# Kernel tuning notes

Hardware: AMD Instinct MI355X
Metric: run time of the kernel (lower is better)

Reference implementation:

```python
import jax, jax.numpy as jnp
import numpy as np

DIM = 384
H = 12
HD = DIM // H  # 32
GROUPS = 6
K = 7
EPS = 1e-5


def layernorm(x, g, b):
    m = x.mean(-1, keepdims=True)
    v = x.var(-1, keepdims=True)
    return (x - m) * jax.lax.rsqrt(v + EPS) * g + b


def setup_inputs() -> dict:
    key = jax.random.key(0)
    ks = jax.random.split(key, 12)
    B, S = 8, 4096
    s = 0.02
    inp = {
        "x": jax.random.normal(ks[0], (B, S, DIM), jnp.float32),
        # grouped Conv1d: weight (out=384, in_per_group=64, k=7)
        "conv_w": jax.random.normal(ks[1], (DIM, DIM // GROUPS, K), jnp.float32) * s,
        "conv_b": jnp.zeros((DIM,), jnp.float32),
        "q_w": jax.random.normal(ks[2], (DIM, DIM), jnp.float32) * s,
        "q_b": jnp.zeros((DIM,), jnp.float32),
        "k_w": jax.random.normal(ks[3], (DIM, DIM), jnp.float32) * s,
        "k_b": jnp.zeros((DIM,), jnp.float32),
        "v_w": jax.random.normal(ks[4], (DIM, DIM), jnp.float32) * s,
        "v_b": jnp.zeros((DIM,), jnp.float32),
        "g_w": jax.random.normal(ks[5], (DIM, DIM), jnp.float32) * s,
        "g_b": jnp.zeros((DIM,), jnp.float32),
        "decay": jnp.ones((1, H, 1, HD), jnp.float32) * 0.85,
        "ln1_g": jnp.ones((DIM,), jnp.float32),
        "ln1_b": jnp.zeros((DIM,), jnp.float32),
        "w1": jax.random.normal(ks[6], (DIM, 2 * DIM), jnp.float32) * s,
        "b1": jnp.zeros((2 * DIM,), jnp.float32),
        "w2": jax.random.normal(ks[7], (2 * DIM, DIM), jnp.float32) * s,
        "b2": jnp.zeros((DIM,), jnp.float32),
        "ln2_g": jnp.ones((DIM,), jnp.float32),
        "ln2_b": jnp.zeros((DIM,), jnp.float32),
    }
    return inp


def reference(x, conv_w, conv_b, q_w, q_b, k_w, k_b, v_w, v_b, g_w, g_b,
              decay, ln1_g, ln1_b, w1, b1, w2, b2, ln2_g, ln2_b):
    b, s, d = x.shape
    # grouped depth-blocked conv over time (torch Conv1d, pad=3, groups=6)
    xc = jax.lax.conv_general_dilated(
        x.transpose(0, 2, 1), conv_w, window_strides=(1,), padding=((3, 3),),
        feature_group_count=GROUPS, dimension_numbers=("NCH", "OIH", "NCH"))
    xc = (xc + conv_b[None, :, None]).transpose(0, 2, 1)
    xc = jax.nn.silu(xc)

    def heads(y):  # (b,s,d) -> (b,h,s,hd)
        return y.reshape(b, s, H, HD).transpose(0, 2, 1, 3)

    q = heads(xc @ q_w + q_b)
    k = heads(xc @ k_w + k_b)
    v = heads(xc @ v_w + v_b)
    g = heads(jax.nn.sigmoid(xc @ g_w + g_b))
    v_gated = v * g

    # Fallback recurrence: state = state * mean(sigmoid(decay)) + v_t (x) k_t;
    # output reads only diag(state) -> collapses to a per-dim decayed cumsum of v*k.
    lam = jnp.mean(jax.nn.sigmoid(decay))  # scalar (mean over h,d of expanded w)
    u = v_gated * k                        # (b,h,s,hd)
    u_t = u.transpose(2, 0, 1, 3)          # (s,b,h,hd)

    def step(carry, ut):
        c = carry * lam + ut
        return c, c

    _, diag = jax.lax.scan(step, jnp.zeros((b, H, HD), x.dtype), u_t)
    out = q * diag.transpose(1, 2, 0, 3)   # (b,h,s,hd)

    x_mem = out.transpose(0, 2, 1, 3).reshape(b, s, d)
    h = layernorm(x_mem, ln1_g, ln1_b)
    h = jax.nn.silu(h @ w1 + b1) @ w2 + b2
    return layernorm(h + x, ln2_g, ln2_b)
```

## Files before the change

kernel.cpp:

```cpp
#include <hip/hip_runtime.h>
#include <hip/hip_bf16.h>

#define DIMD 384
#define SEQL 4096
#define NBATCH 8
#define NTOK (NBATCH*SEQL)

typedef float f32x4 __attribute__((ext_vector_type(4)));
typedef short s16x8 __attribute__((ext_vector_type(8)));
typedef unsigned short u16;
typedef __hip_bfloat16 bf16;

__device__ __forceinline__ float sigf(float x){ return 1.f/(1.f+__expf(-x)); }

typedef __attribute__((address_space(3))) void lds_void;
typedef const __attribute__((address_space(1))) void glb_void;
__device__ __forceinline__ void gl_lds16(const void* g, void* l) {
  __builtin_amdgcn_global_load_lds((glb_void*)g, (lds_void*)l, 16, 0, 0);
}

#define OFF_LAM   0ul
#define OFF_WQ    4096ul
#define OFF_CW    (OFF_WQ + 1179648ul)
#define OFF_W1T   (OFF_CW + 344064ul)
#define OFF_W2T   (OFF_W1T + 589824ul)
#define OFF_XC    4194304ul
#define OFF_Q     (OFF_XC + 25165824ul)
#define OFF_U     (OFF_XC + 50331648ul)
#define OFF_AI    OFF_U
#define OFF_H     (OFF_U + 50331648ul)

__global__ void k_prep_w(const float* __restrict__ qw, const float* __restrict__ kw,
                         const float* __restrict__ vw, const float* __restrict__ gw,
                         const float* __restrict__ cw, const float* __restrict__ w1,
                         const float* __restrict__ w2,
                         bf16* __restrict__ wqt, bf16* __restrict__ cwt,
                         bf16* __restrict__ w1t, bf16* __restrict__ w2t) {
  const int total = 589824 + 172032 + 294912 + 294912;
  for (int j = blockIdx.x*blockDim.x + threadIdx.x; j < total; j += gridDim.x*blockDim.x) {
    if (j < 589824) {
      int n = j / 384, k = j % 384;
      int mat = n / 384;
      int np = n % 384;
      const float* W = (mat==0)?qw:(mat==1)?kw:(mat==2)?vw:gw;
      wqt[(size_t)n*384 + k] = __float2bfloat16(W[(size_t)k*384 + np]);
    } else if (j < 589824 + 172032) {
      int jj = j - 589824;
      int o = jj / 448, k = jj % 448;
      int kap = k >> 6, i = k & 63;
      cwt[(size_t)o*448 + k] = __float2bfloat16(cw[((size_t)o*64 + i)*7 + kap]);
    } else if (j < 589824 + 172032 + 294912) {
      int jj = j - (589824 + 172032);
      int n = jj / 384, k = jj % 384;
      w1t[(size_t)n*384 + k] = __float2bfloat16(w1[(size_t)k*768 + n]);
    } else {
      int jj = j - (589824 + 172032 + 294912);
      int n = jj / 768, k = jj % 768;
      w2t[(size_t)n*768 + k] = __float2bfloat16(w2[(size_t)k*384 + n]);
    }
  }
}

__global__ void k_prep_lam(const float* __restrict__ decay, float* __restrict__ lam) {
  __shared__ float red[6];
  int t = threadIdx.x;
  float v = sigf(decay[t]);
  for (int off = 32; off; off >>= 1) v += __shfl_xor(v, off, 64);
  if ((t & 63) == 0) red[t >> 6] = v;
  __syncthreads();
  if (t == 0) {
    float s = 0.f;
    for (int i = 0; i < 6; ++i) s += red[i];
    lam[0] = s * (1.f/384.f);
  }
}

__global__ __launch_bounds__(256) void k_conv(const float* __restrict__ x, const float* __restrict__ cb,
                                              const bf16* __restrict__ cwt, bf16* __restrict__ xc) {
  int id = blockIdx.x;
  int g = id % 6, st = (id/6) & 31, b = id / 192;
  int s0 = st * 128;
  __shared__ u16 xls[134*72];
  __shared__ u16 wls[64*456];
  int tid = threadIdx.x;
  for (int r0 = 0; r0 < 144; r0 += 16) {
    int row = r0 + (tid >> 4);
    if (row < 134) {
      int col = (tid & 15) * 4;
      int s = s0 - 3 + row;
      float4 v = make_float4(0.f,0.f,0.f,0.f);
      if (s >= 0 && s < SEQL)
        v = *reinterpret_cast<const float4*>(x + ((size_t)(b*SEQL + s))*DIMD + g*64 + col);
      u16* dst = &xls[row*72 + col];
      bf16 t0 = __float2bfloat16(v.x); dst[0] = *reinterpret_cast<u16*>(&t0);
      bf16 t1 = __float2bfloat16(v.y); dst[1] = *reinterpret_cast<u16*>(&t1);
      bf16 t2 = __float2bfloat16(v.z); dst[2] = *reinterpret_cast<u16*>(&t2);
      bf16 t3 = __float2bfloat16(v.w); dst[3] = *reinterpret_cast<u16*>(&t3);
    }
  }
  for (int i0 = 0; i0 < 28672; i0 += 1024) {
    int i = i0 + tid*4;
    int o = i / 448, k = i % 448;
    *reinterpret_cast<uint2*>(&wls[o*456 + k]) =
      *reinterpret_cast<const uint2*>(cwt + ((size_t)(g*64 + o))*448 + k);
  }
  __syncthreads();
  int w = tid >> 6, l = tid & 63, l15 = l & 15, lh = l >> 4;
  f32x4 zz = {0.f,0.f,0.f,0.f};
  f32x4 acc[2][4];
  for (int i=0;i<2;++i) for (int jn=0;jn<4;++jn) acc[i][jn]=zz;
  for (int kap = 0; kap < 7; ++kap) {
#pragma unroll
    for (int ic = 0; ic < 2; ++ic) {
      s16x8 a0 = *reinterpret_cast<const s16x8*>(&xls[(w*32 +  0 + l15 + kap)*72 + ic*32 + lh*8]);
      s16x8 a1 = *reinterpret_cast<const s16x8*>(&xls[(w*32 + 16 + l15 + kap)*72 + ic*32 + lh*8]);
#pragma unroll
      for (int nf = 0; nf < 4; ++nf) {
        s16x8 bfr = *reinterpret_cast<const s16x8*>(&wls[(nf*16 + l15)*456 + kap*64 + ic*32 + lh*8]);
        acc[0][nf] = __builtin_amdgcn_mfma_f32_16x16x32_bf16(a0, bfr, acc[0][nf], 0,0,0);
        acc[1][nf] = __builtin_amdgcn_mfma_f32_16x16x32_bf16(a1, bfr, acc[1][nf], 0,0,0);
      }
    }
  }
#pragma unroll
  for (int nf = 0; nf < 4; ++nf) {
    int ch = g*64 + nf*16 + l15;
    float bias = cb[ch];
#pragma unroll
    for (int mf = 0; mf < 2; ++mf) {
#pragma unroll
      for (int r = 0; r < 4; ++r) {
        int m = w*32 + mf*16 + lh*4 + r;
        float v = acc[mf][nf][r] + bias;
        v = v * sigf(v);
        xc[((size_t)(b*SEQL + s0 + m))*DIMD + ch] = __float2bfloat16(v);
      }
    }
  }
}

__global__ __launch_bounds__(256) void k_qkvg(const bf16* __restrict__ xc, const bf16* __restrict__ wt,
    const float* __restrict__ qb, const float* __restrict__ kb,
    const float* __restrict__ vb, const float* __restrict__ gb,
    bf16* __restrict__ qout, bf16* __restrict__ uout) {
  int raw = blockIdx.x;
  int vv = (raw & 7)*384 + (raw >> 3);
  int mt = vv / 12, ct = vv % 12;
  int m0 = mt*128, c0 = ct*32;
  __shared__ __align__(16) u16 smem[16384];
  u16* als = smem;
  int tid = threadIdx.x, w = tid >> 6, l = tid & 63, l15 = l & 15, lh = l >> 4;
  f32x4 zz = {0.f,0.f,0.f,0.f};
  f32x4 acc[8][2];
#pragma unroll
  for (int i=0;i<8;++i){ acc[i][0]=zz; acc[i][1]=zz; }
  const bf16* b0p = wt + ((size_t)(w*384 + c0 + l15))*384 + lh*8;
  const bf16* b1p = b0p + (size_t)16*384;
  for (int kc = 0; kc < 3; ++kc) {
#pragma unroll
    for (int p = 0; p < 8; ++p) {
      int off16 = p*256 + tid;
      int row = off16 >> 4, slot = off16 & 15;
      int sslot = slot ^ (row & 7);
      gl_lds16(xc + ((size_t)(m0+row))*DIMD + kc*128 + sslot*8,
               (char*)als + off16*16);
    }
    __syncthreads();
#pragma unroll
    for (int kk = 0; kk < 4; ++kk) {
      int ko = kc*128 + kk*32;
      s16x8 bf0 = *reinterpret_cast<const s16x8*>(b0p + ko);
      s16x8 bf1 = *reinterpret_cast<const s16x8*>(b1p + ko);
#pragma unroll
      for (int mf = 0; mf < 8; ++mf) {
        s16x8 af = *reinterpret_cast<const s16x8*>(
            &als[(mf*16 + l15)*128 + (((kk*4 + lh) ^ (l15 & 7))*8)]);
        acc[mf][0] = __builtin_amdgcn_mfma_f32_16x16x32_bf16(af, bf0, acc[mf][0], 0,0,0);
        acc[mf][1] = __builtin_amdgcn_mfma_f32_16x16x32_bf16(af, bf1, acc[mf][1], 0,0,0);
      }
    }
    __syncthreads();
  }
  const float* bp = (w==0)?qb:(w==1)?kb:(w==2)?vb:gb;
  float bias0 = bp[c0 + l15], bias1 = bp[c0 + 16 + l15];
  if (w == 0) {
#pragma unroll
    for (int mf=0;mf<8;++mf)
#pragma unroll
      for (int nf=0;nf<2;++nf) {
        float bs = nf ? bias1 : bias0;
#pragma unroll
        for (int r=0;r<4;++r) {
          int m = mf*16 + lh*4 + r, c = nf*16 + l15;
          qout[((size_t)(m0+m))*DIMD + c0 + c] = __float2bfloat16(acc[mf][nf][r] + bs);
        }
      }
  } else {
    u16* exm = smem + (size_t)(w-1)*(128*40);
#pragma unroll
    for (int mf=0;mf<8;++mf)
#pragma unroll
      for (int nf=0;nf<2;++nf) {
        float bs = nf ? bias1 : bias0;
#pragma unroll
        for (int r=0;r<4;++r) {
          int m = mf*16 + lh*4 + r, c = nf*16 + l15;
          bf16 t = __float2bfloat16(acc[mf][nf][r] + bs);
          exm[m*40 + c] = *reinterpret_cast<u16*>(&t);
        }
      }
  }
  __syncthreads();
#pragma unroll
  for (int p = 0; p < 16; ++p) {
    int idx = p*256 + tid;
    int m = idx >> 5, c = idx & 31;
    u16 kr = smem[0*(128*40) + m*40 + c];
    u16 vr = smem[1*(128*40) + m*40 + c];
    u16 gr = smem[2*(128*40) + m*40 + c];
    float kvv = __bfloat162float(*reinterpret_cast<bf16*>(&kr));
    float vvv = __bfloat162float(*reinterpret_cast<bf16*>(&vr));
    float gvv = __bfloat162float(*reinterpret_cast<bf16*>(&gr));
    uout[((size_t)(m0+m))*DIMD + c0 + c] = __float2bfloat16(vvv * sigf(gvv) * kvv);
  }
}

__global__ __launch_bounds__(384) void k_scan(const bf16* __restrict__ u, const bf16* __restrict__ q,
    const float* __restrict__ lam_p, const float* __restrict__ l1g, const float* __restrict__ l1b,
    bf16* __restrict__ h) {
  int b = blockIdx.x >> 5, c = blockIdx.x & 31;
  int d = threadIdx.x;
  float lam = lam_p[0];
  __shared__ float ols[64*384];
  __shared__ float lgs[384], lbs[384];
  lgs[d] = l1g[d]; lbs[d] = l1b[d];
  int s0 = c*128;
  size_t base = ((size_t)b*SEQL)*DIMD + d;
  float carry = 0.f;
  int sstart = s0 - 64; if (sstart < 0) sstart = 0;
  for (int s = sstart; s < s0; s += 8) {
    float uv[8];
#pragma unroll
    for (int j = 0; j < 8; ++j) uv[j] = __bfloat162float(u[base + (size_t)(s+j)*DIMD]);
#pragma unroll
    for (int j = 0; j < 8; ++j) carry = carry*lam + uv[j];
  }
  int w = d >> 6, lane = d & 63;
  for (int p = 0; p < 2; ++p) {
    int sb = s0 + p*64;
    __syncthreads();
    for (int it0 = 0; it0 < 64; it0 += 8) {
      float uv[8], qv[8];
#pragma unroll
      for (int j = 0; j < 8; ++j) uv[j] = __bfloat162float(u[base + (size_t)(sb+it0+j)*DIMD]);
#pragma unroll
      for (int j = 0; j < 8; ++j) qv[j] = __bfloat162float(q[base + (size_t)(sb+it0+j)*DIMD]);
#pragma unroll
      for (int j = 0; j < 8; ++j) {
        carry = carry*lam + uv[j];
        ols[(it0+j)*384 + d] = carry * qv[j];
      }
    }
    __syncthreads();
    for (int t = w; t < 64; t += 6) {
      float vv[6]; float s1 = 0.f, s2 = 0.f;
#pragma unroll
      for (int j = 0; j < 6; ++j) {
        vv[j] = ols[t*384 + j*64 + lane];
        s1 += vv[j]; s2 += vv[j]*vv[j];
      }
      for (int off = 32; off; off >>= 1) { s1 += __shfl_xor(s1, off, 64); s2 += __shfl_xor(s2, off, 64); }
      float mean = s1 * (1.f/384.f);
      float var = s2 * (1.f/384.f) - mean*mean;
      float rs = rsqrtf(var + 1e-5f);
      size_t rowo = ((size_t)(b*SEQL + sb + t))*DIMD;
#pragma unroll
      for (int j = 0; j < 6; ++j) {
        int dd = j*64 + lane;
        h[rowo + dd] = __float2bfloat16((vv[j]-mean)*rs*lgs[dd] + lbs[dd]);
      }
    }
  }
}

__global__ __launch_bounds__(256) void k_mlp1(const bf16* __restrict__ h, const bf16* __restrict__ w1t,
                                              const float* __restrict__ b1, bf16* __restrict__ ai) {
  int raw = blockIdx.x;
  int vv = (raw & 7)*192 + (raw >> 3);
  int mt = vv / 6, nt = vv % 6;
  int m0 = mt*128, n0 = nt*128;
  __shared__ __align__(16) u16 als[16384];
  int tid = threadIdx.x, w = tid >> 6, l = tid & 63, l15 = l & 15, lh = l >> 4;
  int wm = (w >> 1)*64, wn = (w & 1)*64;
  f32x4 zz = {0.f,0.f,0.f,0.f};
  f32x4 acc[4][4];
#pragma unroll
  for (int i=0;i<4;++i) for (int jn=0;jn<4;++jn) acc[i][jn]=zz;
  const bf16* bp0 = w1t + ((size_t)(n0 + wn + l15))*384 + lh*8;
  for (int kc = 0; kc < 3; ++kc) {
#pragma unroll
    for (int p = 0; p < 8; ++p) {
      int off16 = p*256 + tid;
      int row = off16 >> 4, slot = off16 & 15;
      int sslot = slot ^ (row & 7);
      gl_lds16(h + ((size_t)(m0+row))*DIMD + kc*128 + sslot*8,
               (char*)als + off16*16);
    }
    __syncthreads();
#pragma unroll
    for (int kk = 0; kk < 4; ++kk) {
      int ko = kc*128 + kk*32;
      s16x8 bfr[4];
#pragma unroll
      for (int nf = 0; nf < 4; ++nf)
        bfr[nf] = *reinterpret_cast<const s16x8*>(bp0 + (size_t)nf*16*384 + ko);
#pragma unroll
      for (int mf = 0; mf < 4; ++mf) {
        s16x8 af = *reinterpret_cast<const s16x8*>(
            &als[(wm + mf*16 + l15)*128 + (((kk*4 + lh) ^ (l15 & 7))*8)]);
#pragma unroll
        for (int nf = 0; nf < 4; ++nf)
          acc[mf][nf] = __builtin_amdgcn_mfma_f32_16x16x32_bf16(af, bfr[nf], acc[mf][nf], 0,0,0);
      }
    }
    __syncthreads();
  }
  float bias[4];
#pragma unroll
  for (int nf = 0; nf < 4; ++nf) bias[nf] = b1[n0 + wn + nf*16 + l15];
#pragma unroll
  for (int mf = 0; mf < 4; ++mf)
#pragma unroll
    for (int nf = 0; nf < 4; ++nf)
#pragma unroll
      for (int r = 0; r < 4; ++r) {
        int m = wm + mf*16 + lh*4 + r, ch = n0 + wn + nf*16 + l15;
        float v = acc[mf][nf][r] + bias[nf];
        v = v * sigf(v);
        ai[(size_t)(m0+m)*768 + ch] = __float2bfloat16(v);
      }
}

__global__ __launch_bounds__(256) void k_mlp2ln(const bf16* __restrict__ ai, const bf16* __restrict__ w2t,
                                                const float* __restrict__ b2, const float* __restrict__ x,
                                                const float* __restrict__ l2g, const float* __restrict__ l2b,
                                                float* __restrict__ out) {
  int raw = blockIdx.x;
  int mt = (raw & 7)*128 + (raw >> 3);
  int m0 = mt*32;
  __shared__ __align__(16) u16 als[4096];
  __shared__ float pls[4][32][2];
  int tid = threadIdx.x, w = tid >> 6, l = tid & 63, l15 = l & 15, lh = l >> 4;
  int wn = w*96;
  f32x4 zz = {0.f,0.f,0.f,0.f};
  f32x4 acc[2][6];
#pragma unroll
  for (int i=0;i<2;++i)
#pragma unroll
    for (int jn=0;jn<6;++jn) acc[i][jn]=zz;
  const bf16* bp0 = w2t + ((size_t)(wn + l15))*768 + lh*8;
  for (int kc = 0; kc < 6; ++kc) {
#pragma unroll
    for (int p = 0; p < 2; ++p) {
      int off16 = p*256 + tid;
      int row = off16 >> 4, slot = off16 & 15;
      int sslot = slot ^ (row & 7);
      gl_lds16(ai + ((size_t)(m0+row))*768 + kc*128 + sslot*8,
               (char*)als + off16*16);
    }
    __syncthreads();
#pragma unroll
    for (int kk = 0; kk < 4; ++kk) {
      int ko = kc*128 + kk*32;
      s16x8 bfr[6];
#pragma unroll
      for (int nf = 0; nf < 6; ++nf)
        bfr[nf] = *reinterpret_cast<const s16x8*>(bp0 + (size_t)nf*16*768 + ko);
#pragma unroll
      for (int mf = 0; mf < 2; ++mf) {
        s16x8 af = *reinterpret_cast<const s16x8*>(
            &als[(mf*16 + l15)*128 + (((kk*4 + lh) ^ (l15 & 7))*8)]);
#pragma unroll
        for (int nf = 0; nf < 6; ++nf)
          acc[mf][nf] = __builtin_amdgcn_mfma_f32_16x16x32_bf16(af, bfr[nf], acc[mf][nf], 0,0,0);
      }
    }
    __syncthreads();
  }
  float bias[6];
#pragma unroll
  for (int nf = 0; nf < 6; ++nf) bias[nf] = b2[wn + nf*16 + l15];
#pragma unroll
  for (int mf = 0; mf < 2; ++mf) {
#pragma unroll
    for (int r = 0; r < 4; ++r) {
      int m = mf*16 + lh*4 + r;
      const float* xr = x + (size_t)(m0+m)*DIMD + wn + l15;
      float sa = 0.f, sb = 0.f;
#pragma unroll
      for (int nf = 0; nf < 6; ++nf) {
        float v = acc[mf][nf][r] + bias[nf] + xr[nf*16];
        acc[mf][nf][r] = v;
        sa += v; sb += v*v;
      }
#pragma unroll
      for (int off = 1; off < 16; off <<= 1) {
        sa += __shfl_xor(sa, off, 16);
        sb += __shfl_xor(sb, off, 16);
      }
      if (l15 == 0) { pls[w][m][0] = sa; pls[w][m][1] = sb; }
    }
  }
  __syncthreads();
  float lg[6], lb[6];
#pragma unroll
  for (int nf = 0; nf < 6; ++nf) { lg[nf] = l2g[wn + nf*16 + l15]; lb[nf] = l2b[wn + nf*16 + l15]; }
#pragma unroll
  for (int mf = 0; mf < 2; ++mf) {
#pragma unroll
    for (int r = 0; r < 4; ++r) {
      int m = mf*16 + lh*4 + r;
      float S1 = pls[0][m][0] + pls[1][m][0] + pls[2][m][0] + pls[3][m][0];
      float S2 = pls[0][m][1] + pls[1][m][1] + pls[2][m][1] + pls[3][m][1];
      float mean = S1 * (1.f/384.f);
      float var = S2 * (1.f/384.f) - mean*mean;
      float rs = rsqrtf(var + 1e-5f);
      float* orow = out + (size_t)(m0+m)*DIMD + wn + l15;
#pragma unroll
      for (int nf = 0; nf < 6; ++nf)
        orow[nf*16] = (acc[mf][nf][r] - mean)*rs*lg[nf] + lb[nf];
    }
  }
}

extern "C" void kernel_launch(void* const* d_in, const int* in_sizes, int n_in,
                              void* d_out, int out_size, void* d_ws, size_t ws_size,
                              hipStream_t stream) {
  const float* x   = (const float*)d_in[0];
  const float* cw  = (const float*)d_in[1];
  const float* cb  = (const float*)d_in[2];
  const float* qw  = (const float*)d_in[3];
  const float* qb  = (const float*)d_in[4];
  const float* kw  = (const float*)d_in[5];
  const float* kb  = (const float*)d_in[6];
  const float* vw  = (const float*)d_in[7];
  const float* vb  = (const float*)d_in[8];
  const float* gw  = (const float*)d_in[9];
  const float* gb  = (const float*)d_in[10];
  const float* dec = (const float*)d_in[11];
  const float* l1g = (const float*)d_in[12];
  const float* l1b = (const float*)d_in[13];
  const float* w1  = (const float*)d_in[14];
  const float* b1  = (const float*)d_in[15];
  const float* w2  = (const float*)d_in[16];
  const float* b2  = (const float*)d_in[17];
  const float* l2g = (const float*)d_in[18];
  const float* l2b = (const float*)d_in[19];

  char* ws = (char*)d_ws;
  float* lam = (float*)(ws + OFF_LAM);
  bf16* wqt  = (bf16*)(ws + OFF_WQ);
  bf16* cwt  = (bf16*)(ws + OFF_CW);
  bf16* w1t  = (bf16*)(ws + OFF_W1T);
  bf16* w2t  = (bf16*)(ws + OFF_W2T);
  bf16* xc   = (bf16*)(ws + OFF_XC);
  bf16* q    = (bf16*)(ws + OFF_Q);
  bf16* u    = (bf16*)(ws + OFF_U);
  bf16* hbuf = (bf16*)(ws + OFF_H);
  bf16* ai   = (bf16*)(ws + OFF_AI);
  float* out = (float*)d_out;

  hipLaunchKernelGGL(k_prep_w,  dim3(1024), dim3(256), 0, stream, qw,kw,vw,gw,cw,w1,w2, wqt,cwt,w1t,w2t);
  hipLaunchKernelGGL(k_prep_lam,dim3(1),    dim3(384), 0, stream, dec, lam);
  hipLaunchKernelGGL(k_conv,    dim3(1536), dim3(256), 0, stream, x, cb, cwt, xc);
  hipLaunchKernelGGL(k_qkvg,    dim3(3072), dim3(256), 0, stream, xc, wqt, qb,kb,vb,gb, q, u);
  hipLaunchKernelGGL(k_scan,    dim3(256),  dim3(384), 0, stream, u, q, lam, l1g, l1b, hbuf);
  hipLaunchKernelGGL(k_mlp1,    dim3(1536), dim3(256), 0, stream, hbuf, w1t, b1, ai);
  hipLaunchKernelGGL(k_mlp2ln,  dim3(1024), dim3(256), 0, stream, ai, w2t, b2, x, l2g, l2b, out);
}
```

Before: 264.9 us.

## Fuse MLP up-projection and down-projection+LayerNorm into one kernel via LDS

Merges the two MLP GEMM kernels into a single 512-thread kernel. Each block loads a 32-row tile of the normalized activations into LDS, computes the 768-wide SiLU intermediate into padded LDS, then runs the second GEMM with residual and LayerNorm. This removes the global write and re-read of the 32768x768 bf16 intermediate and one launch. In exchange each block recomputes nothing but uses roughly 74KB LDS, which limits occupancy, and the first GEMM now uses a small 32-row M tile, so W1 is re-read from cache by every block.

Result: slower. 275.5 us (+4.0%).

```diff
diff --git a/kernel.cpp b/kernel.cpp
--- a/kernel.cpp
+++ b/kernel.cpp
@@ -27,7 +27,6 @@
 #define OFF_XC    4194304ul
 #define OFF_Q     (OFF_XC + 25165824ul)
 #define OFF_U     (OFF_XC + 50331648ul)
-#define OFF_AI    OFF_U
 #define OFF_H     (OFF_U + 50331648ul)
 
 __global__ void k_prep_w(const float* __restrict__ qw, const float* __restrict__ kw,
@@ -283,124 +282,108 @@
   }
 }
 
-__global__ __launch_bounds__(256) void k_mlp1(const bf16* __restrict__ h, const bf16* __restrict__ w1t,
-                                              const float* __restrict__ b1, bf16* __restrict__ ai) {
-  int raw = blockIdx.x;
-  int vv = (raw & 7)*192 + (raw >> 3);
-  int mt = vv / 6, nt = vv % 6;
-  int m0 = mt*128, n0 = nt*128;
-  __shared__ __align__(16) u16 als[16384];
-  int tid = threadIdx.x, w = tid >> 6, l = tid & 63, l15 = l & 15, lh = l >> 4;
-  int wm = (w >> 1)*64, wn = (w & 1)*64;
-  f32x4 zz = {0.f,0.f,0.f,0.f};
-  f32x4 acc[4][4];
-#pragma unroll
-  for (int i=0;i<4;++i) for (int jn=0;jn<4;++jn) acc[i][jn]=zz;
-  const bf16* bp0 = w1t + ((size_t)(n0 + wn + l15))*384 + lh*8;
-  for (int kc = 0; kc < 3; ++kc) {
-#pragma unroll
-    for (int p = 0; p < 8; ++p) {
-      int off16 = p*256 + tid;
-      int row = off16 >> 4, slot = off16 & 15;
-      int sslot = slot ^ (row & 7);
-      gl_lds16(h + ((size_t)(m0+row))*DIMD + kc*128 + sslot*8,
-               (char*)als + off16*16);
-    }
-    __syncthreads();
-#pragma unroll
-    for (int kk = 0; kk < 4; ++kk) {
-      int ko = kc*128 + kk*32;
-      s16x8 bfr[4];
-#pragma unroll
-      for (int nf = 0; nf < 4; ++nf)
-        bfr[nf] = *reinterpret_cast<const s16x8*>(bp0 + (size_t)nf*16*384 + ko);
-#pragma unroll
-      for (int mf = 0; mf < 4; ++mf) {
-        s16x8 af = *reinterpret_cast<const s16x8*>(
-            &als[(wm + mf*16 + l15)*128 + (((kk*4 + lh) ^ (l15 & 7))*8)]);
-#pragma unroll
-        for (int nf = 0; nf < 4; ++nf)
-          acc[mf][nf] = __builtin_amdgcn_mfma_f32_16x16x32_bf16(af, bfr[nf], acc[mf][nf], 0,0,0);
-      }
-    }
-    __syncthreads();
-  }
-  float bias[4];
-#pragma unroll
-  for (int nf = 0; nf < 4; ++nf) bias[nf] = b1[n0 + wn + nf*16 + l15];
-#pragma unroll
-  for (int mf = 0; mf < 4; ++mf)
-#pragma unroll
-    for (int nf = 0; nf < 4; ++nf)
-#pragma unroll
-      for (int r = 0; r < 4; ++r) {
-        int m = wm + mf*16 + lh*4 + r, ch = n0 + wn + nf*16 + l15;
-        float v = acc[mf][nf][r] + bias[nf];
-        v = v * sigf(v);
-        ai[(size_t)(m0+m)*768 + ch] = __float2bfloat16(v);
-      }
-}
-
-__global__ __launch_bounds__(256) void k_mlp2ln(const bf16* __restrict__ ai, const bf16* __restrict__ w2t,
-                                                const float* __restrict__ b2, const float* __restrict__ x,
-                                                const float* __restrict__ l2g, const float* __restrict__ l2b,
-                                                float* __restrict__ out) {
+__global__ __launch_bounds__(512) void k_mlp(const bf16* __restrict__ h, const bf16* __restrict__ w1t,
+    const float* __restrict__ b1, const bf16* __restrict__ w2t, const float* __restrict__ b2,
+    const float* __restrict__ x, const float* __restrict__ l2g, const float* __restrict__ l2b,
+    float* __restrict__ out) {
   int raw = blockIdx.x;
   int mt = (raw & 7)*128 + (raw >> 3);
   int m0 = mt*32;
-  __shared__ __align__(16) u16 als[4096];
-  __shared__ float pls[4][32][2];
+  __shared__ __align__(16) u16 hls[12288];
+  __shared__ __align__(16) u16 ails[24832];
+  __shared__ float pls[8][32][2];
   int tid = threadIdx.x, w = tid >> 6, l = tid & 63, l15 = l & 15, lh = l >> 4;
-  int wn = w*96;
+#pragma unroll
+  for (int p = 0; p < 3; ++p) {
+    int off16 = p*512 + tid;
+    int row = off16 / 48, cb = off16 % 48;
+    int scb = cb ^ (row & 7);
+    gl_lds16(h + (size_t)(m0+row)*DIMD + scb*8, (char*)hls + off16*16);
+  }
+  __syncthreads();
   f32x4 zz = {0.f,0.f,0.f,0.f};
-  f32x4 acc[2][6];
+  int wn1 = w*96;
+  {
+    f32x4 acc1[2][6];
+#pragma unroll
+    for (int i=0;i<2;++i)
+#pragma unroll
+      for (int jn=0;jn<6;++jn) acc1[i][jn]=zz;
+    const bf16* bp1 = w1t + ((size_t)(wn1 + l15))*384 + lh*8;
+    for (int kc = 0; kc < 3; ++kc) {
+#pragma unroll
+      for (int kk = 0; kk < 4; ++kk) {
+        int ko = kc*128 + kk*32;
+        s16x8 bfr[6];
+#pragma unroll
+        for (int nf = 0; nf < 6; ++nf)
+          bfr[nf] = *reinterpret_cast<const s16x8*>(bp1 + (size_t)nf*16*384 + ko);
+#pragma unroll
+        for (int mf = 0; mf < 2; ++mf) {
+          int row = mf*16 + l15;
+          int cb = kc*16 + kk*4 + lh;
+          s16x8 af = *reinterpret_cast<const s16x8*>(&hls[row*384 + ((cb ^ (row & 7))*8)]);
+#pragma unroll
+          for (int nf = 0; nf < 6; ++nf)
+            acc1[mf][nf] = __builtin_amdgcn_mfma_f32_16x16x32_bf16(af, bfr[nf], acc1[mf][nf], 0,0,0);
+        }
+      }
+    }
+    float bias1[6];
+#pragma unroll
+    for (int nf = 0; nf < 6; ++nf) bias1[nf] = b1[wn1 + nf*16 + l15];
+#pragma unroll
+    for (int mf = 0; mf < 2; ++mf)
+#pragma unroll
+      for (int nf = 0; nf < 6; ++nf)
+#pragma unroll
+        for (int r = 0; r < 4; ++r) {
+          int m = mf*16 + lh*4 + r, ch = wn1 + nf*16 + l15;
+          float v = acc1[mf][nf][r] + bias1[nf];
+          v = v * sigf(v);
+          bf16 t = __float2bfloat16(v);
+          ails[m*776 + ch] = *reinterpret_cast<u16*>(&t);
+        }
+  }
+  __syncthreads();
+  int wn2 = w*48;
+  f32x4 acc2[2][3];
 #pragma unroll
   for (int i=0;i<2;++i)
 #pragma unroll
-    for (int jn=0;jn<6;++jn) acc[i][jn]=zz;
-  const bf16* bp0 = w2t + ((size_t)(wn + l15))*768 + lh*8;
+    for (int jn=0;jn<3;++jn) acc2[i][jn]=zz;
+  const bf16* bp2 = w2t + ((size_t)(wn2 + l15))*768 + lh*8;
   for (int kc = 0; kc < 6; ++kc) {
-#pragma unroll
-    for (int p = 0; p < 2; ++p) {
-      int off16 = p*256 + tid;
-      int row = off16 >> 4, slot = off16 & 15;
-      int sslot = slot ^ (row & 7);
-      gl_lds16(ai + ((size_t)(m0+row))*768 + kc*128 + sslot*8,
-               (char*)als + off16*16);
-    }
-    __syncthreads();
 #pragma unroll
     for (int kk = 0; kk < 4; ++kk) {
       int ko = kc*128 + kk*32;
-      s16x8 bfr[6];
-#pragma unroll
-      for (int nf = 0; nf < 6; ++nf)
-        bfr[nf] = *reinterpret_cast<const s16x8*>(bp0 + (size_t)nf*16*768 + ko);
+      s16x8 bfr[3];
+#pragma unroll
+      for (int nf = 0; nf < 3; ++nf)
+        bfr[nf] = *reinterpret_cast<const s16x8*>(bp2 + (size_t)nf*16*768 + ko);
 #pragma unroll
       for (int mf = 0; mf < 2; ++mf) {
-        s16x8 af = *reinterpret_cast<const s16x8*>(
-            &als[(mf*16 + l15)*128 + (((kk*4 + lh) ^ (l15 & 7))*8)]);
-#pragma unroll
-        for (int nf = 0; nf < 6; ++nf)
-          acc[mf][nf] = __builtin_amdgcn_mfma_f32_16x16x32_bf16(af, bfr[nf], acc[mf][nf], 0,0,0);
-      }
-    }
-    __syncthreads();
-  }
-  float bias[6];
-#pragma unroll
-  for (int nf = 0; nf < 6; ++nf) bias[nf] = b2[wn + nf*16 + l15];
+        s16x8 af = *reinterpret_cast<const s16x8*>(&ails[(mf*16 + l15)*776 + ko + lh*8]);
+#pragma unroll
+        for (int nf = 0; nf < 3; ++nf)
+          acc2[mf][nf] = __builtin_amdgcn_mfma_f32_16x16x32_bf16(af, bfr[nf], acc2[mf][nf], 0,0,0);
+      }
+    }
+  }
+  float bias2[3];
+#pragma unroll
+  for (int nf = 0; nf < 3; ++nf) bias2[nf] = b2[wn2 + nf*16 + l15];
 #pragma unroll
   for (int mf = 0; mf < 2; ++mf) {
 #pragma unroll
     for (int r = 0; r < 4; ++r) {
       int m = mf*16 + lh*4 + r;
-      const float* xr = x + (size_t)(m0+m)*DIMD + wn + l15;
+      const float* xr = x + (size_t)(m0+m)*DIMD + wn2 + l15;
       float sa = 0.f, sb = 0.f;
 #pragma unroll
-      for (int nf = 0; nf < 6; ++nf) {
-        float v = acc[mf][nf][r] + bias[nf] + xr[nf*16];
-        acc[mf][nf][r] = v;
+      for (int nf = 0; nf < 3; ++nf) {
+        float v = acc2[mf][nf][r] + bias2[nf] + xr[nf*16];
+        acc2[mf][nf][r] = v;
         sa += v; sb += v*v;
       }
 #pragma unroll
@@ -412,23 +395,24 @@
     }
   }
   __syncthreads();
-  float lg[6], lb[6];
-#pragma unroll
-  for (int nf = 0; nf < 6; ++nf) { lg[nf] = l2g[wn + nf*16 + l15]; lb[nf] = l2b[wn + nf*16 + l15]; }
+  float lg[3], lb[3];
+#pragma unroll
+  for (int nf = 0; nf < 3; ++nf) { lg[nf] = l2g[wn2 + nf*16 + l15]; lb[nf] = l2b[wn2 + nf*16 + l15]; }
 #pragma unroll
   for (int mf = 0; mf < 2; ++mf) {
 #pragma unroll
     for (int r = 0; r < 4; ++r) {
       int m = mf*16 + lh*4 + r;
-      float S1 = pls[0][m][0] + pls[1][m][0] + pls[2][m][0] + pls[3][m][0];
-      float S2 = pls[0][m][1] + pls[1][m][1] + pls[2][m][1] + pls[3][m][1];
+      float S1 = 0.f, S2 = 0.f;
+#pragma unroll
+      for (int ww = 0; ww < 8; ++ww) { S1 += pls[ww][m][0]; S2 += pls[ww][m][1]; }
       float mean = S1 * (1.f/384.f);
       float var = S2 * (1.f/384.f) - mean*mean;
       float rs = rsqrtf(var + 1e-5f);
-      float* orow = out + (size_t)(m0+m)*DIMD + wn + l15;
-#pragma unroll
-      for (int nf = 0; nf < 6; ++nf)
-        orow[nf*16] = (acc[mf][nf][r] - mean)*rs*lg[nf] + lb[nf];
+      float* orow = out + (size_t)(m0+m)*DIMD + wn2 + l15;
+#pragma unroll
+      for (int nf = 0; nf < 3; ++nf)
+        orow[nf*16] = (acc2[mf][nf][r] - mean)*rs*lg[nf] + lb[nf];
     }
   }
 }
@@ -467,7 +451,6 @@
   bf16* q    = (bf16*)(ws + OFF_Q);
   bf16* u    = (bf16*)(ws + OFF_U);
   bf16* hbuf = (bf16*)(ws + OFF_H);
-  bf16* ai   = (bf16*)(ws + OFF_AI);
   float* out = (float*)d_out;
 
   hipLaunchKernelGGL(k_prep_w,  dim3(1024), dim3(256), 0, stream, qw,kw,vw,gw,cw,w1,w2, wqt,cwt,w1t,w2t);
@@ -475,6 +458,5 @@
   hipLaunchKernelGGL(k_conv,    dim3(1536), dim3(256), 0, stream, x, cb, cwt, xc);
   hipLaunchKernelGGL(k_qkvg,    dim3(3072), dim3(256), 0, stream, xc, wqt, qb,kb,vb,gb, q, u);
   hipLaunchKernelGGL(k_scan,    dim3(256),  dim3(384), 0, stream, u, q, lam, l1g, l1b, hbuf);
-  hipLaunchKernelGGL(k_mlp1,    dim3(1536), dim3(256), 0, stream, hbuf, w1t, b1, ai);
-  hipLaunchKernelGGL(k_mlp2ln,  dim3(1024), dim3(256), 0, stream, ai, w2t, b2, x, l2g, l2b, out);
-}
+  hipLaunchKernelGGL(k_mlp,     dim3(1024), dim3(512), 0, stream, hbuf, w1t, b1, w2t, b2, x, l2g, l2b, out);
+}
```
